# Kernel tuning notes

Hardware: AMD Instinct MI355X
Metric: run time of the kernel (lower is better)

The kernel has to match this reference:

```python
import jax, jax.numpy as jnp
import numpy as np

EMBED_DIM_LIST = [256, 512]
NUM_HEADS_LIST = [4, 8]
MAX_EMBED = 512
N_BASE = 8                       # = max(num_heads_list)
MAX_HS = max(EMBED_DIM_LIST) // min(NUM_HEADS_LIST)  # 128


def _config_masks():
    # One {0,1} mask per (emb, heads) config, shape [n_cfg, N_BASE, MAX_HS, MAX_EMBED].
    # Mask encodes: slice base weight [:head_size, :emb], zero-pad to (MAX_HS, MAX_EMBED),
    # and that only the first `heads` base heads receive a contribution.
    r = np.arange(MAX_HS)[:, None]
    c = np.arange(MAX_EMBED)[None, :]
    masks = []
    for emb in EMBED_DIM_LIST:
        for heads in NUM_HEADS_LIST:
            hs = emb // heads
            m2 = ((r < hs) & (c < emb)).astype(np.float32)      # [MAX_HS, MAX_EMBED]
            hm = (np.arange(N_BASE) < heads).astype(np.float32)  # [N_BASE]
            masks.append(hm[:, None, None] * m2[None])
    return jnp.asarray(np.stack(masks))  # [4, 8, 128, 512]

_CFG_MASKS = _config_masks()


def setup_inputs() -> dict:
    key = jax.random.key(0)
    k0, k1, k2, k3, k4 = jax.random.split(key, 5)
    B, T = 4, 2048
    x = jax.random.normal(k0, (B, T, MAX_EMBED), dtype=jnp.float32)
    weights = jax.random.uniform(k1, (len(EMBED_DIM_LIST) * len(NUM_HEADS_LIST),), dtype=jnp.float32)
    s = 0.02
    base_K = jax.random.normal(k2, (N_BASE, MAX_HS, MAX_EMBED), dtype=jnp.float32) * s
    base_Q = jax.random.normal(k3, (N_BASE, MAX_HS, MAX_EMBED), dtype=jnp.float32) * s
    base_V = jax.random.normal(k4, (N_BASE, MAX_HS, MAX_EMBED), dtype=jnp.float32) * s
    return {"x": x, "weights": weights, "base_K": base_K, "base_Q": base_Q, "base_V": base_V}


def reference(x, weights, base_K, base_Q, base_V):
    B, T, C = x.shape
    # Weight mixing: sum_i weights[i] * (padded slice of base weight) for each base head.
    eff = jnp.einsum('i,ihde->hde', weights, _CFG_MASKS)  # [H, MAX_HS, MAX_EMBED]
    Wk = eff * base_K
    Wq = eff * base_Q
    Wv = eff * base_V
    # Projections for all base heads at once: F.linear(x, W) == x @ W.T
    k = jnp.einsum('btc,hdc->bhtd', x, Wk)
    q = jnp.einsum('btc,hdc->bhtd', x, Wq)
    v = jnp.einsum('btc,hdc->bhtd', x, Wv)
    # Causal self-attention; scale uses k.shape[-1] == MAX_HS (padded head size), as in source.
    scale = 1.0 / jnp.sqrt(jnp.asarray(MAX_HS, dtype=x.dtype))
    att = jnp.einsum('bhtd,bhsd->bhts', q, k) * scale       # [B, H, T, T]
    tril = jnp.tril(jnp.ones((T, T), dtype=bool))
    att = jnp.where(tril, att, -jnp.inf)
    wei = jax.nn.softmax(att, axis=-1)                       # dropout = identity (eval)
    out = jnp.einsum('bhts,bhsd->bhtd', wei, v)              # [B, H, T, MAX_HS]
    # torch.cat(head_out_list, dim=-1) in head order == transpose + reshape
    return out.transpose(0, 2, 1, 3).reshape(B, T, N_BASE * MAX_HS)
```

## Files before the change

### kernel.cpp

```cpp
#include <hip/hip_runtime.h>
#include <hip/hip_bf16.h>
#include <stdint.h>

typedef __attribute__((ext_vector_type(8))) short bf16x8;
typedef __attribute__((ext_vector_type(4))) float f32x4;
typedef __attribute__((ext_vector_type(16))) float f32x16;

#define MFMA16(a,b,c) __builtin_amdgcn_mfma_f32_16x16x32_bf16((a),(b),(c),0,0,0)
#define MFMA32(a,b,c) __builtin_amdgcn_mfma_f32_32x32x16_bf16((a),(b),(c),0,0,0)
#define AS1 __attribute__((address_space(1)))
#define AS3 __attribute__((address_space(3)))

__device__ inline short f2bf(float f) {
    union { __hip_bfloat16 h; short s; } u;
    u.h = __float2bfloat16(f);
    return u.s;
}
__device__ inline uint32_t pack_bf16(float a, float b) {
    union { __hip_bfloat16 h; uint16_t u; } ua, ub;
    ua.h = __float2bfloat16(a); ub.h = __float2bfloat16(b);
    return (uint32_t)ua.u | ((uint32_t)ub.u << 16);
}

#if __has_builtin(__builtin_amdgcn_permlane32_swap)
#define SWAP32(x, y, a, b) { auto _r = __builtin_amdgcn_permlane32_swap((a),(b),false,false); \
                             (x) = _r[0]; (y) = _r[1]; }
#else
#define SWAP32(x, y, a, b) { uint32_t _ta = __shfl_xor((uint32_t)(a),32); \
                             uint32_t _tb = __shfl_xor((uint32_t)(b),32); \
                             (x) = hh_ ? _tb : (a); (y) = hh_ ? (b) : _ta; }
#endif

#define QSCALE 0.12751879523879295f

#define NW (8*128*512)
#define NX4 (8192*512/4)

__global__ void prep_kernel(const float* __restrict__ x,
                            const float* __restrict__ w,
                            const float* __restrict__ bK,
                            const float* __restrict__ bQ,
                            const float* __restrict__ bV,
                            short* __restrict__ xb,
                            short* __restrict__ W)
{
    const float w0 = w[0], w1 = w[1], w2 = w[2], w3 = w[3];
    for (int i = blockIdx.x * blockDim.x + threadIdx.x; i < NW + NX4;
         i += gridDim.x * blockDim.x) {
        if (i < NW) {
            int e = i & 511;
            int d = (i >> 9) & 127;
            int h = i >> 16;
            float eff = 0.f;
            if (h < 4) { eff += w2; if (d < 64 && e < 256) eff += w0; }
            if (d < 32 && e < 256) eff += w1;
            if (d < 64) eff += w3;
            W[i]          = f2bf(eff * bK[i]);
            W[i + NW]     = f2bf(eff * bQ[i] * QSCALE);
            W[i + 2*NW]   = f2bf(eff * bV[i]);
        } else {
            int j = i - NW;
            float4 v = ((const float4*)x)[j];
            short4 o;
            o.x = f2bf(v.x); o.y = f2bf(v.y); o.z = f2bf(v.z); o.w = f2bf(v.w);
            ((short4*)xb)[j] = o;
        }
    }
}

__global__ __launch_bounds__(256)
void proj_gemm(const short* __restrict__ A,
               const short* __restrict__ Bw,
               short* __restrict__ qkv)
{
    __shared__ short S[128 * 128];
    short* As = S;
    short* Bs = S + 128 * 64;
    const int tid = threadIdx.x;
    const int lane = tid & 63;
    const int wave = tid >> 6;
    const int wr = wave >> 1, wc = wave & 1;
    const int l15 = lane & 15, lk = lane >> 4;

    const int wg = (blockIdx.x & 7) * 192 + (blockIdx.x >> 3);
    const int bm = (wg / 24) * 128;
    const int bn = (wg % 24) * 128;

    char* Ab = (char*)As;
    char* Bb = (char*)Bs;
    char* Sb = (char*)S;
    f32x4 acc[4][4] = {};

    for (int k0 = 0; k0 < 512; k0 += 64) {
        __syncthreads();
#pragma unroll
        for (int i = 0; i < 4; ++i) {
            int c = i * 256 + tid;
            int lin = c * 16;
            int row = lin >> 7;
            int cof = ((lin & 127) ^ ((row & 7) << 4)) >> 1;
            __builtin_amdgcn_global_load_lds(
                (const AS1 void*)(A + (size_t)(bm + row) * 512 + k0 + cof),
                (AS3 void*)(As + c * 8), 16, 0, 0);
            __builtin_amdgcn_global_load_lds(
                (const AS1 void*)(Bw + (size_t)(bn + row) * 512 + k0 + cof),
                (AS3 void*)(Bs + c * 8), 16, 0, 0);
        }
        __syncthreads();
#pragma unroll
        for (int kk = 0; kk < 2; ++kk) {
            bf16x8 af[4], bfv[4];
#pragma unroll
            for (int mi = 0; mi < 4; ++mi) {
                int row = wr * 64 + mi * 16 + l15;
                af[mi] = *(const bf16x8*)(Ab + ((row * 128 + kk * 64 + lk * 16) ^ ((row & 7) << 4)));
            }
#pragma unroll
            for (int ni = 0; ni < 4; ++ni) {
                int row = wc * 64 + ni * 16 + l15;
                bfv[ni] = *(const bf16x8*)(Bb + ((row * 128 + kk * 64 + lk * 16) ^ ((row & 7) << 4)));
            }
#pragma unroll
            for (int mi = 0; mi < 4; ++mi)
#pragma unroll
                for (int ni = 0; ni < 4; ++ni)
                    acc[mi][ni] = MFMA16(af[mi], bfv[ni], acc[mi][ni]);
        }
    }

    const int proj = bn >> 10;
    const int b = bm >> 11;
    const int bh = b * 8 + ((bn & 1023) >> 7);
    const int tbase = bm & 2047;

    __syncthreads();
    if (proj == 2) {
#pragma unroll
        for (int mi = 0; mi < 4; ++mi) {
#pragma unroll
            for (int ni = 0; ni < 4; ++ni) {
                int dl = wc * 64 + ni * 16 + l15;
                int tlb = wr * 64 + mi * 16 + lk * 4;
                int byte0 = (dl * 256 + tlb * 2) ^ ((dl & 7) << 4);
                *(uint32_t*)(Sb + byte0)     = pack_bf16(acc[mi][ni][0], acc[mi][ni][1]);
                *(uint32_t*)(Sb + byte0 + 4) = pack_bf16(acc[mi][ni][2], acc[mi][ni][3]);
            }
        }
    } else {
#pragma unroll
        for (int mi = 0; mi < 4; ++mi) {
#pragma unroll
            for (int ni = 0; ni < 4; ++ni) {
                int dl = wc * 64 + ni * 16 + l15;
#pragma unroll
                for (int r = 0; r < 4; ++r) {
                    int tl = wr * 64 + mi * 16 + lk * 4 + r;
                    *(short*)(Sb + ((tl * 256 + dl * 2) ^ ((tl & 7) << 4))) = f2bf(acc[mi][ni][r]);
                }
            }
        }
    }
    __syncthreads();

    short* dst;
    if (proj == 2)
        dst = qkv + (size_t)2 * (32 * 2048 * 128) + (size_t)bh * 128 * 2048;
    else
        dst = qkv + (size_t)proj * (32 * 2048 * 128) + (size_t)bh * 2048 * 128;

#pragma unroll
    for (int i = 0; i < 8; ++i) {
        int c = i * 256 + tid;
        int row = c >> 4;
        uint4 v = *(const uint4*)(Sb + row * 256 + (((c & 15) * 16) ^ ((row & 7) << 4)));
        if (proj == 2) {
            *(uint4*)(dst + (size_t)row * 2048 + tbase + (c & 15) * 8) = v;
        } else {
            *(uint4*)(dst + (size_t)(tbase + row) * 128 + (c & 15) * 8) = v;
        }
    }
}

__device__ inline void stage_tile(const short* __restrict__ Kp,
                                  const short* __restrict__ Vp,
                                  char* smem, int buf)
{
    short* kls = (short*)(smem + (buf << 14));
    short* vls = (short*)(smem + 32768 + (buf << 14));
    const int tid = threadIdx.x;
#pragma unroll
    for (int i = 0; i < 4; ++i) {
        int c = i * 256 + tid;
        int lin = c * 16;
        int rk = lin >> 8;
        int kof = ((lin & 255) ^ ((rk & 15) << 4)) >> 1;
        __builtin_amdgcn_global_load_lds(
            (const AS1 void*)(Kp + (size_t)rk * 128 + kof),
            (AS3 void*)(kls + c * 8), 16, 0, 0);
        int rv = lin >> 8;
        int p = (lin & 255) ^ ((rv & 15) << 4);
        int d = rv * 2 + (p >> 7);
        int t = (p & 127) >> 1;
        __builtin_amdgcn_global_load_lds(
            (const AS1 void*)(Vp + (size_t)d * 2048 + t),
            (AS3 void*)(vls + c * 8), 16, 0, 0);
    }
}

__global__ __launch_bounds__(256, 2)
void attn_kernel(const short* __restrict__ qkv, float* __restrict__ out)
{
    extern __shared__ char smem[];
    const int tid = threadIdx.x, lane = tid & 63, wave = tid >> 6;
    const int l31 = lane & 31;
    const int hh_ = lane >> 5;

    const int bh = blockIdx.x & 31;
    const int s = 31 - (blockIdx.x >> 5);
    const int q0 = s * 64;

    const int qw = wave & 1;
    const int kvh = wave >> 1;
    const int kvoff = kvh * 32;

    const size_t HSTRIDE = (size_t)2048 * 128;
    const short* Kp = qkv + (size_t)bh * HSTRIDE;
    const short* Qp = qkv + (size_t)32 * HSTRIDE + (size_t)bh * HSTRIDE;
    const short* Vp = qkv + (size_t)64 * HSTRIDE + (size_t)bh * 128 * 2048;

    bf16x8 qf[8];
    {
        const short* qrow = Qp + (size_t)(q0 + qw * 32 + l31) * 128 + hh_ * 8;
#pragma unroll
        for (int dblk = 0; dblk < 8; ++dblk)
            qf[dblk] = *(const bf16x8*)(qrow + dblk * 16);
    }

    float mrow = -1e30f, lrow = 0.f;
    f32x16 acco[4] = {};

    const int ntiles = s + 1;
    const int qwave = q0 + qw * 32;
    const int qglob = qwave + l31;

    stage_tile(Kp, Vp, smem, 0);
    int cur = 0;

    for (int jt = 0; jt < ntiles; ++jt) {
        const int j0 = jt * 64;
        __builtin_amdgcn_s_barrier();
        if (jt + 1 < ntiles) {
            stage_tile(Kp + (size_t)(j0 + 64) * 128, Vp + (j0 + 64),
                       smem, cur ^ 1);
            asm volatile("s_waitcnt vmcnt(8)" ::: "memory");
        } else {
            asm volatile("s_waitcnt vmcnt(0)" ::: "memory");
        }
        __builtin_amdgcn_sched_barrier(0);
        __builtin_amdgcn_s_barrier();
        __builtin_amdgcn_sched_barrier(0);

        const int kv0 = j0 + kvoff;
        if (kv0 <= qwave + 31) {
            char* Kb = smem + (cur << 14);
            char* Vb = smem + 32768 + (cur << 14);

            f32x16 sacc = {};
            __builtin_amdgcn_s_setprio(1);
#pragma unroll
            for (int dblk = 0; dblk < 8; ++dblk) {
                int row = kvoff + l31;
                bf16x8 kf = *(const bf16x8*)(Kb + ((row * 256 + dblk * 32 + hh_ * 16) ^ ((row & 15) << 4)));
                sacc = MFMA32(kf, qf[dblk], sacc);
            }
            __builtin_amdgcn_s_setprio(0);

            if (kv0 + 31 > qwave) {
#pragma unroll
                for (int r = 0; r < 16; ++r) {
                    int kvglob = kv0 + (r & 3) + 8 * (r >> 2) + 4 * hh_;
                    if (kvglob > qglob) sacc[r] = -1e30f;
                }
            }

            float pmax = -1e30f;
#pragma unroll
            for (int r = 0; r < 16; r += 4) {
                float a = fmaxf(sacc[r], sacc[r + 1]);
                float b2 = fmaxf(sacc[r + 2], sacc[r + 3]);
                pmax = fmaxf(pmax, fmaxf(a, b2));
            }
            pmax = fmaxf(pmax, __shfl_xor(pmax, 32));

            if (!__all(pmax - mrow <= 11.5416f)) {
                float mn = fmaxf(mrow, pmax);
                float alpha = __builtin_amdgcn_exp2f(mrow - mn);
                mrow = mn;
                lrow *= alpha;
#pragma unroll
                for (int r = 0; r < 16; ++r) {
                    float ar = __shfl(alpha, (r & 3) + 8 * (r >> 2) + 4 * hh_);
#pragma unroll
                    for (int dt = 0; dt < 4; ++dt) acco[dt][r] *= ar;
                }
            }

            float psum = 0.f;
            uint32_t pkA[4], pkB[4];
#pragma unroll
            for (int sg = 0; sg < 4; ++sg) {
                float p0 = __builtin_amdgcn_exp2f(sacc[4 * sg + 0] - mrow);
                float p1 = __builtin_amdgcn_exp2f(sacc[4 * sg + 1] - mrow);
                float p2 = __builtin_amdgcn_exp2f(sacc[4 * sg + 2] - mrow);
                float p3 = __builtin_amdgcn_exp2f(sacc[4 * sg + 3] - mrow);
                psum += (p0 + p1) + (p2 + p3);
                pkA[sg] = pack_bf16(p0, p1);
                pkB[sg] = pack_bf16(p2, p3);
            }
            psum += __shfl_xor(psum, 32);
            lrow += psum;

            __builtin_amdgcn_s_setprio(1);
#pragma unroll
            for (int kbl = 0; kbl < 2; ++kbl) {
                uint32_t r0, r1, r2, r3;
                SWAP32(r0, r2, pkA[2 * kbl], pkA[2 * kbl + 1]);
                SWAP32(r1, r3, pkB[2 * kbl], pkB[2 * kbl + 1]);
                union { uint32_t u[4]; bf16x8 v; } pa;
                pa.u[0] = r0; pa.u[1] = r1; pa.u[2] = r2; pa.u[3] = r3;
                const int kb = kvh * 2 + kbl;
#pragma unroll
                for (int dt = 0; dt < 4; ++dt) {
                    int d = dt * 32 + l31;
                    int r = d >> 1;
                    int inner = ((d & 1) << 7) + kb * 32 + hh_ * 16;
                    bf16x8 vf = *(const bf16x8*)(Vb + (r * 256 + (inner ^ ((r & 15) << 4))));
                    acco[dt] = MFMA32(pa.v, vf, acco[dt]);
                }
            }
            __builtin_amdgcn_s_setprio(0);
        }

        cur ^= 1;
    }

    __syncthreads();
    float* ex = (float*)smem;
    float* ml = (float*)(smem + 32768);
    if (kvh == 1) {
        float* dst = ex + qw * 4096;
#pragma unroll
        for (int dt = 0; dt < 4; ++dt)
#pragma unroll
            for (int r = 0; r < 16; ++r)
                dst[(dt * 16 + r) * 64 + lane] = acco[dt][r];
        ml[qw * 128 + lane * 2 + 0] = mrow;
        ml[qw * 128 + lane * 2 + 1] = lrow;
    }
    __syncthreads();
    if (kvh == 0) {
        float m1 = ml[qw * 128 + lane * 2 + 0];
        float l1 = ml[qw * 128 + lane * 2 + 1];
        float M  = fmaxf(mrow, m1);
        float a  = __builtin_amdgcn_exp2f(mrow - M);
        float b2 = __builtin_amdgcn_exp2f(m1 - M);
        float lf = lrow * a + l1 * b2;
        float sA = a / lf, sB = b2 / lf;
        const float* src = ex + qw * 4096;
        const int b = bh >> 3, hd = bh & 7;
#pragma unroll
        for (int r = 0; r < 16; ++r) {
            int ql = (r & 3) + 8 * (r >> 2) + 4 * hh_;
            float sa = __shfl(sA, ql);
            float sb = __shfl(sB, ql);
            int t = qwave + ql;
            float* o = out + (size_t)(b * 2048 + t) * 1024 + hd * 128 + l31;
#pragma unroll
            for (int dt = 0; dt < 4; ++dt)
                o[dt * 32] = acco[dt][r] * sa + src[(dt * 16 + r) * 64 + lane] * sb;
        }
    }
}

extern "C" void kernel_launch(void* const* d_in, const int* in_sizes, int n_in,
                              void* d_out, int out_size, void* d_ws, size_t ws_size,
                              hipStream_t stream) {
    const float* x  = (const float*)d_in[0];
    const float* w  = (const float*)d_in[1];
    const float* bK = (const float*)d_in[2];
    const float* bQ = (const float*)d_in[3];
    const float* bV = (const float*)d_in[4];

    short* xb  = (short*)d_ws;
    short* W   = (short*)((char*)d_ws + 8388608);
    short* qkv = (short*)((char*)d_ws + 8388608 + 3145728);
    float* out = (float*)d_out;

    hipFuncSetAttribute((const void*)attn_kernel,
                        hipFuncAttributeMaxDynamicSharedMemorySize, 65536);

    prep_kernel<<<2048, 256, 0, stream>>>(x, w, bK, bQ, bV, xb, W);
    proj_gemm<<<64 * 24, 256, 0, stream>>>(xb, W, qkv);
    attn_kernel<<<32 * 32, 256, 65536, stream>>>(qkv, out);
}
```

Measured before the change: 106.6 us.

## Use 32-row KV tiles with 4-stage prefetch ring and MFMA-friendly LDS layout

```diff
diff --git a/kernel.cpp b/kernel.cpp
--- a/kernel.cpp
+++ b/kernel.cpp
@@ -181,28 +181,27 @@
     }
 }
 
-__device__ inline void stage_tile(const short* __restrict__ Kp,
-                                  const short* __restrict__ Vp,
-                                  char* smem, int buf)
+__device__ inline void stage_tile32(const short* __restrict__ Kp,
+                                    const short* __restrict__ Vp,
+                                    int j0, char* smem, int buf)
 {
     short* kls = (short*)(smem + (buf << 14));
-    short* vls = (short*)(smem + 32768 + (buf << 14));
+    short* vls = kls + 4096;
     const int tid = threadIdx.x;
 #pragma unroll
-    for (int i = 0; i < 4; ++i) {
+    for (int i = 0; i < 2; ++i) {
         int c = i * 256 + tid;
-        int lin = c * 16;
-        int rk = lin >> 8;
-        int kof = ((lin & 255) ^ ((rk & 15) << 4)) >> 1;
+        int slot = c >> 5, t = c & 31;
         __builtin_amdgcn_global_load_lds(
-            (const AS1 void*)(Kp + (size_t)rk * 128 + kof),
+            (const AS1 void*)(Kp + (size_t)(j0 + t) * 128 + slot * 8),
             (AS3 void*)(kls + c * 8), 16, 0, 0);
-        int rv = lin >> 8;
-        int p = (lin & 255) ^ ((rv & 15) << 4);
-        int d = rv * 2 + (p >> 7);
-        int t = (p & 127) >> 1;
+    }
+#pragma unroll
+    for (int i = 0; i < 2; ++i) {
+        int c = i * 256 + tid;
+        int slot = c >> 7, d = c & 127;
         __builtin_amdgcn_global_load_lds(
-            (const AS1 void*)(Vp + (size_t)d * 2048 + t),
+            (const AS1 void*)(Vp + (size_t)d * 2048 + j0 + slot * 8),
             (AS3 void*)(vls + c * 8), 16, 0, 0);
     }
 }
@@ -215,18 +214,19 @@
     const int l31 = lane & 31;
     const int hh_ = lane >> 5;
 
-    const int bh = blockIdx.x & 31;
-    const int s = 31 - (blockIdx.x >> 5);
-    const int q0 = s * 64;
+    const int x = blockIdx.x & 7;
+    const int g = blockIdx.x >> 3;
+    const int bh = x * 4 + (g & 3);
+    const int sp = 31 - (g >> 2);
+    const int q0 = sp * 64;
 
     const int qw = wave & 1;
-    const int kvh = wave >> 1;
-    const int kvoff = kvh * 32;
+    const int kvp = wave >> 1;
 
     const size_t HSTRIDE = (size_t)2048 * 128;
     const short* Kp = qkv + (size_t)bh * HSTRIDE;
     const short* Qp = qkv + (size_t)32 * HSTRIDE + (size_t)bh * HSTRIDE;
-    const short* Vp = qkv + (size_t)64 * HSTRIDE + (size_t)bh * 128 * 2048;
+    const short* Vp = qkv + (size_t)64 * HSTRIDE + (size_t)bh * HSTRIDE;
 
     bf16x8 qf[8];
     {
@@ -239,20 +239,24 @@
     float mrow = -1e30f, lrow = 0.f;
     f32x16 acco[4] = {};
 
-    const int ntiles = s + 1;
+    const int nt = 2 * sp + 2;
     const int qwave = q0 + qw * 32;
     const int qglob = qwave + l31;
 
-    stage_tile(Kp, Vp, smem, 0);
-    int cur = 0;
-
-    for (int jt = 0; jt < ntiles; ++jt) {
-        const int j0 = jt * 64;
+    stage_tile32(Kp, Vp, 0,  smem, 0);
+    stage_tile32(Kp, Vp, 32, smem, 1);
+    stage_tile32(Kp, Vp, 64, smem, 2);
+
+    for (int jt = 0; jt < nt; ++jt) {
+        const int j0 = jt << 5;
         __builtin_amdgcn_s_barrier();
-        if (jt + 1 < ntiles) {
-            stage_tile(Kp + (size_t)(j0 + 64) * 128, Vp + (j0 + 64),
-                       smem, cur ^ 1);
+        if (jt + 3 < nt) {
+            stage_tile32(Kp, Vp, (jt + 3) << 5, smem, (jt + 3) & 3);
+            asm volatile("s_waitcnt vmcnt(12)" ::: "memory");
+        } else if (jt == nt - 3) {
             asm volatile("s_waitcnt vmcnt(8)" ::: "memory");
+        } else if (jt == nt - 2) {
+            asm volatile("s_waitcnt vmcnt(4)" ::: "memory");
         } else {
             asm volatile("s_waitcnt vmcnt(0)" ::: "memory");
         }
@@ -260,25 +264,23 @@
         __builtin_amdgcn_s_barrier();
         __builtin_amdgcn_sched_barrier(0);
 
-        const int kv0 = j0 + kvoff;
-        if (kv0 <= qwave + 31) {
-            char* Kb = smem + (cur << 14);
-            char* Vb = smem + 32768 + (cur << 14);
+        if (((jt & 1) == kvp) && (j0 <= qwave)) {
+            const short* kls = (const short*)(smem + ((jt & 3) << 14));
+            const short* vls = kls + 4096;
 
             f32x16 sacc = {};
             __builtin_amdgcn_s_setprio(1);
 #pragma unroll
             for (int dblk = 0; dblk < 8; ++dblk) {
-                int row = kvoff + l31;
-                bf16x8 kf = *(const bf16x8*)(Kb + ((row * 256 + dblk * 32 + hh_ * 16) ^ ((row & 15) << 4)));
+                bf16x8 kf = *(const bf16x8*)(kls + dblk * 512 + hh_ * 256 + l31 * 8);
                 sacc = MFMA32(kf, qf[dblk], sacc);
             }
             __builtin_amdgcn_s_setprio(0);
 
-            if (kv0 + 31 > qwave) {
+            if (j0 == qwave) {
 #pragma unroll
                 for (int r = 0; r < 16; ++r) {
-                    int kvglob = kv0 + (r & 3) + 8 * (r >> 2) + 4 * hh_;
+                    int kvglob = j0 + (r & 3) + 8 * (r >> 2) + 4 * hh_;
                     if (kvglob > qglob) sacc[r] = -1e30f;
                 }
             }
@@ -322,32 +324,26 @@
 
             __builtin_amdgcn_s_setprio(1);
 #pragma unroll
-            for (int kbl = 0; kbl < 2; ++kbl) {
+            for (int kb = 0; kb < 2; ++kb) {
                 uint32_t r0, r1, r2, r3;
-                SWAP32(r0, r2, pkA[2 * kbl], pkA[2 * kbl + 1]);
-                SWAP32(r1, r3, pkB[2 * kbl], pkB[2 * kbl + 1]);
+                SWAP32(r0, r2, pkA[2 * kb], pkA[2 * kb + 1]);
+                SWAP32(r1, r3, pkB[2 * kb], pkB[2 * kb + 1]);
                 union { uint32_t u[4]; bf16x8 v; } pa;
                 pa.u[0] = r0; pa.u[1] = r1; pa.u[2] = r2; pa.u[3] = r3;
-                const int kb = kvh * 2 + kbl;
 #pragma unroll
                 for (int dt = 0; dt < 4; ++dt) {
-                    int d = dt * 32 + l31;
-                    int r = d >> 1;
-                    int inner = ((d & 1) << 7) + kb * 32 + hh_ * 16;
-                    bf16x8 vf = *(const bf16x8*)(Vb + (r * 256 + (inner ^ ((r & 15) << 4))));
+                    bf16x8 vf = *(const bf16x8*)(vls + (kb * 2 + hh_) * 1024 + (dt * 32 + l31) * 8);
                     acco[dt] = MFMA32(pa.v, vf, acco[dt]);
                 }
             }
             __builtin_amdgcn_s_setprio(0);
         }
-
-        cur ^= 1;
     }
 
     __syncthreads();
     float* ex = (float*)smem;
     float* ml = (float*)(smem + 32768);
-    if (kvh == 1) {
+    if (kvp == 1) {
         float* dst = ex + qw * 4096;
 #pragma unroll
         for (int dt = 0; dt < 4; ++dt)
@@ -358,7 +354,7 @@
         ml[qw * 128 + lane * 2 + 1] = lrow;
     }
     __syncthreads();
-    if (kvh == 0) {
+    if (kvp == 0) {
         float m1 = ml[qw * 128 + lane * 2 + 0];
         float l1 = ml[qw * 128 + lane * 2 + 1];
         float M  = fmaxf(mrow, m1);
```

Measured after the change: 135.6 us. 27.2% more time.
